# Kernel optimization log

Measured on AMD Instinct MI355X. Metric: run time of the kernel, lower is better.

## Reference

```python
import jax, jax.numpy as jnp
import numpy as np
import math

TANH_CLIP = 10.0
NEG_INF = -100000000.0

def setup_inputs() -> dict:
    key = jax.random.key(0)
    k1, k2, k3, k4, k5 = jax.random.split(key, 5)
    B, Nq, Nk, D = 64, 1024, 1024, 256
    scale = 1.0 / math.sqrt(D)  # ~xavier-ish scale for weights
    return {
        "q": jax.random.normal(k1, (B, Nq, D), dtype=jnp.float32),
        "k": jax.random.normal(k2, (B, Nk, D), dtype=jnp.float32),
        "w_query": jax.random.normal(k3, (D, D), dtype=jnp.float32) * scale,
        "w_key": jax.random.normal(k4, (D, D), dtype=jnp.float32) * scale,
        "mask": jax.random.randint(k5, (B, Nq, Nk), 0, 2, dtype=jnp.int32),
    }

def reference(q, k, w_query, w_key, mask):
    D = q.shape[-1]
    norm = 1.0 / math.sqrt(D)  # key_dim == embedding_dim
    Q = jnp.einsum("bqd,de->bqe", q, w_query)  # [B,Nq,D]
    K = jnp.einsum("bkd,de->bke", k, w_key)    # [B,Nk,D]
    U = norm * jnp.einsum("bqe,bke->bqk", Q, K)
    U = TANH_CLIP * jnp.tanh(U)
    U = jnp.where(mask == 1, NEG_INF, U)
    return jax.nn.log_softmax(U, axis=-1)
```

## Files before the change

### kernel.cpp

```cpp
#include <hip/hip_runtime.h>
#include <hip/hip_bf16.h>
#include <stdint.h>

#define NEG_INF -100000000.0f

typedef __attribute__((ext_vector_type(8))) short bf16x8;
typedef __attribute__((ext_vector_type(4))) float f32x4;
typedef __attribute__((ext_vector_type(4))) int i32x4;

#define LGKM_BAR()                                                \
    do {                                                          \
        asm volatile("s_waitcnt lgkmcnt(0)" ::: "memory");        \
        __builtin_amdgcn_s_barrier();                             \
        __builtin_amdgcn_sched_barrier(0);                        \
    } while (0)

static __device__ __forceinline__ short f2bf(float x) {
    unsigned u = __float_as_uint(x);
    u = u + 0x7FFFu + ((u >> 16) & 1u);
    return (short)(u >> 16);
}

__global__ void wtrans_kernel(const float* __restrict__ wq, const float* __restrict__ wk,
                              short* __restrict__ wtq, short* __restrict__ wtk) {
    __shared__ float tile[32][33];
    const float* w = blockIdx.z ? wk : wq;
    short* wt = blockIdx.z ? wtk : wtq;
    float scale = blockIdx.z ? 1.0f : 0.0625f;
    int tx = threadIdx.x, ty = threadIdx.y;
    int c0 = blockIdx.x * 32;
    int k0 = blockIdx.y * 32;
#pragma unroll
    for (int i = 0; i < 4; i++)
        tile[ty + i * 8][tx] = w[(k0 + ty + i * 8) * 256 + c0 + tx];
    __syncthreads();
#pragma unroll
    for (int i = 0; i < 4; i++)
        wt[(c0 + ty + i * 8) * 256 + k0 + tx] = f2bf(tile[tx][ty + i * 8] * scale);
}

__global__ __launch_bounds__(512, 4)
void proj_kernel(const float* __restrict__ qin, const float* __restrict__ kin,
                 const short* __restrict__ wtq, const short* __restrict__ wtk,
                 short* __restrict__ Qb, short* __restrict__ Kb,
                 const int* __restrict__ mask, unsigned* __restrict__ pmask) {
    if (blockIdx.y == 2) {
        int t = threadIdx.x;
        size_t row = (size_t)blockIdx.x * 64 + (t >> 3);
        int seg8 = t & 7;
        const int* mrow = mask + row * 1024;
#pragma unroll
        for (int jj = 0; jj < 4; jj++) {
            int j = seg8 + jj * 8;
            unsigned v = 0;
#pragma unroll
            for (int i = 0; i < 8; i++) {
                i32x4 x = __builtin_nontemporal_load(
                    reinterpret_cast<const i32x4*>(mrow + j * 4 + i * 128));
                unsigned nib = (unsigned)(x.x | (x.y << 1) | (x.z << 2) | (x.w << 3));
                v |= nib << (i * 4);
            }
            pmask[row * 32 + j] = v;
        }
        return;
    }

    const float* x  = blockIdx.y ? kin : qin;
    const short* wt = blockIdx.y ? wtk : wtq;
    short* outp     = blockIdx.y ? Kb  : Qb;

    __shared__ __align__(16) char slds[40960];
    short* xl0 = (short*)slds;
    short* wl0 = xl0 + 2048;
    short* xl1 = (short*)(slds + 20480);
    short* wl1 = xl1 + 2048;

    int t = threadIdx.x;
    int lane = t & 63, w = t >> 6;
    int l15 = lane & 15, g = lane >> 4;
    int rowbase = blockIdx.x * 64;

    int srow = t >> 3, sseg = t & 7;
    const float* xrow = x + (size_t)(rowbase + srow) * 256 + sseg * 4;
    int wc0 = t >> 2, wseg0 = t & 3;
    int wc1 = (512 + t) >> 2, wseg1 = t & 3;

    f32x4 zero = {0.f, 0.f, 0.f, 0.f};
    f32x4 acc[4][2];
#pragma unroll
    for (int m = 0; m < 4; m++)
#pragma unroll
        for (int n = 0; n < 2; n++) acc[m][n] = zero;

    {
        f32x4 xv = __builtin_nontemporal_load(reinterpret_cast<const f32x4*>(xrow));
        int4 wv0 = *reinterpret_cast<const int4*>(wt + wc0 * 256 + wseg0 * 8);
        int4 wv1 = *reinterpret_cast<const int4*>(wt + wc1 * 256 + wseg1 * 8);
        short4 bb; bb.x = f2bf(xv.x); bb.y = f2bf(xv.y); bb.z = f2bf(xv.z); bb.w = f2bf(xv.w);
        *reinterpret_cast<short4*>(&xl0[srow * 32 + sseg * 4]) = bb;
        *reinterpret_cast<int4*>(&wl0[(size_t)t * 8]) = wv0;
        *reinterpret_cast<int4*>(&wl0[((size_t)512 + t) * 8]) = wv1;
    }
    LGKM_BAR();

#pragma unroll
    for (int dc = 0; dc < 8; dc++) {
        short* xc   = (dc & 1) ? xl1 : xl0;
        short* wcur = (dc & 1) ? wl1 : wl0;
        short* xn   = (dc & 1) ? xl0 : xl1;
        short* wn   = (dc & 1) ? wl0 : wl1;

        f32x4 xv; int4 wv0, wv1;
        if (dc < 7) {
            xv  = __builtin_nontemporal_load(reinterpret_cast<const f32x4*>(xrow + (dc + 1) * 32));
            wv0 = *reinterpret_cast<const int4*>(wt + wc0 * 256 + (dc + 1) * 32 + wseg0 * 8);
            wv1 = *reinterpret_cast<const int4*>(wt + wc1 * 256 + (dc + 1) * 32 + wseg1 * 8);
        }

        bf16x8 a[4], bfr[2];
#pragma unroll
        for (int m = 0; m < 4; m++)
            a[m] = *reinterpret_cast<const bf16x8*>(&xc[(m * 16 + l15) * 32 + g * 8]);
#pragma unroll
        for (int n = 0; n < 2; n++) {
            int c = w * 32 + n * 16 + l15;
            bfr[n] = *reinterpret_cast<const bf16x8*>(&wcur[c * 32 + g * 8]);
        }
#pragma unroll
        for (int m = 0; m < 4; m++)
#pragma unroll
            for (int n = 0; n < 2; n++)
                acc[m][n] = __builtin_amdgcn_mfma_f32_16x16x32_bf16(a[m], bfr[n], acc[m][n], 0, 0, 0);

        if (dc < 7) {
            short4 bb; bb.x = f2bf(xv.x); bb.y = f2bf(xv.y); bb.z = f2bf(xv.z); bb.w = f2bf(xv.w);
            *reinterpret_cast<short4*>(&xn[srow * 32 + sseg * 4]) = bb;
            *reinterpret_cast<int4*>(&wn[(size_t)t * 8]) = wv0;
            *reinterpret_cast<int4*>(&wn[((size_t)512 + t) * 8]) = wv1;
            LGKM_BAR();
        }
    }

    LGKM_BAR();
    short* sdump = (short*)slds;
#pragma unroll
    for (int m = 0; m < 4; m++)
#pragma unroll
        for (int n = 0; n < 2; n++) {
            int col = w * 32 + n * 16 + l15;
#pragma unroll
            for (int r = 0; r < 4; r++)
                sdump[(m * 16 + g * 4 + r) * 296 + col] = f2bf(acc[m][n][r]);
        }
    LGKM_BAR();

    int b8 = rowbase >> 10;
    int rloc = rowbase & 1023;
#pragma unroll
    for (int o = 0; o < 4; o++) {
        int gu = o * 512 + t;
        int dc = gu >> 8;
        int rem = gu & 255;
        int row = rem >> 2, kseg = rem & 3;
        int4 v = *reinterpret_cast<const int4*>(&sdump[row * 296 + dc * 32 + kseg * 8]);
        size_t idx = (((size_t)b8 * 8 + dc) * 1024 + rloc + row) * 32 + kseg * 8;
        *reinterpret_cast<int4*>(outp + idx) = v;
    }
}

__global__ __launch_bounds__(512, 4)
void attn_kernel(const short* __restrict__ Qs, const short* __restrict__ Ks,
                 const unsigned* __restrict__ pmask, float* __restrict__ out) {
    const int RSB = 1034;
    __shared__ __align__(16) short ulds0[16 * RSB];
    __shared__ __align__(16) short ulds1[16 * RSB];

    int t = threadIdx.x;
    int lane = t & 63, w = t >> 6;
    int l15 = lane & 15, g = lane >> 4;

    int bid = blockIdx.x;
    int wg = (bid & 7) * 256 + (bid >> 3);
    int b = wg >> 5;
    int brow = (wg & 31) * 32;

    const unsigned* pm = pmask + ((size_t)b * 1024 + brow) * 32;
    unsigned mw0 = pm[t];
    unsigned mw1 = pm[512 + t];

    const short* qb = Qs + (size_t)b * 8 * 32768;
    const short* kb = Ks + (size_t)b * 8 * 32768;

    f32x4 zero = {0.f, 0.f, 0.f, 0.f};
    f32x4 acc[2][8];
#pragma unroll
    for (int m = 0; m < 2; m++)
#pragma unroll
        for (int n = 0; n < 8; n++) acc[m][n] = zero;

    for (int dc = 0; dc < 8; dc++) {
        const short* qc = qb + dc * 32768;
        const short* kc = kb + dc * 32768;
        bf16x8 a0 = *reinterpret_cast<const bf16x8*>(qc + (brow + l15) * 32 + g * 8);
        bf16x8 a1 = *reinterpret_cast<const bf16x8*>(qc + (brow + 16 + l15) * 32 + g * 8);
#pragma unroll
        for (int n = 0; n < 8; n++) {
            bf16x8 bf = *reinterpret_cast<const bf16x8*>(kc + (w * 128 + n * 16 + l15) * 32 + g * 8);
            acc[0][n] = __builtin_amdgcn_mfma_f32_16x16x32_bf16(a0, bf, acc[0][n], 0, 0, 0);
            acc[1][n] = __builtin_amdgcn_mfma_f32_16x16x32_bf16(a1, bf, acc[1][n], 0, 0, 0);
        }
    }

    int prow = t >> 5;
    int j = t & 31;

#pragma unroll
    for (int n = 0; n < 8; n++)
#pragma unroll
        for (int r = 0; r < 4; r++)
            ulds0[(g * 4 + r) * RSB + w * 128 + n * 16 + l15] = f2bf(acc[0][n][r]);
    LGKM_BAR();

#pragma unroll
    for (int n = 0; n < 8; n++)
#pragma unroll
        for (int r = 0; r < 4; r++)
            ulds1[(g * 4 + r) * RSB + w * 128 + n * 16 + l15] = f2bf(acc[1][n][r]);

#pragma unroll
    for (int m = 0; m < 2; m++) {
        short* buf = m ? ulds1 : ulds0;
        unsigned bits = m ? mw1 : mw0;
        short* urow = buf + prow * RSB;

        float psum = 0.f;
#pragma unroll
        for (int i = 0; i < 8; i++) {
            int col = j * 4 + i * 128;
            unsigned lo = *reinterpret_cast<const unsigned*>(&urow[col]);
            unsigned hi = *reinterpret_cast<const unsigned*>(&urow[col + 2]);
            float uv[4] = {__uint_as_float(lo << 16), __uint_as_float(lo & 0xffff0000u),
                           __uint_as_float(hi << 16), __uint_as_float(hi & 0xffff0000u)};
            unsigned short ucb[4];
#pragma unroll
            for (int c = 0; c < 4; c++) {
                float e2 = __expf(2.0f * uv[c]);
                float tc = 10.0f - 20.0f / (e2 + 1.0f);
                bool msk = (bits >> (i * 4 + c)) & 1;
                float uc = msk ? NEG_INF : tc;
                ucb[c] = (unsigned short)f2bf(uc);
                psum += msk ? 0.0f : __expf(tc);
            }
            *reinterpret_cast<unsigned*>(&urow[col]) = (unsigned)ucb[0] | ((unsigned)ucb[1] << 16);
            *reinterpret_cast<unsigned*>(&urow[col + 2]) = (unsigned)ucb[2] | ((unsigned)ucb[3] << 16);
        }
        psum += __shfl_xor(psum, 1);
        psum += __shfl_xor(psum, 2);
        psum += __shfl_xor(psum, 4);
        psum += __shfl_xor(psum, 8);
        psum += __shfl_xor(psum, 16);
        float lse = __logf(fmaxf(psum, 1e-30f));
        float lse0 = __shfl(lse, 0);
        float lse1 = __shfl(lse, 32);

        float* obase = out + ((size_t)b * 1024 + brow + m * 16) * 1024;
#pragma unroll
        for (int rr = 0; rr < 2; rr++) {
            int r2 = w * 2 + rr;
            float lser = rr ? lse1 : lse0;
            const short* ur2 = buf + r2 * RSB;
            float* orow = obase + (size_t)r2 * 1024;
#pragma unroll
            for (int i2 = 0; i2 < 4; i2++) {
                int col = lane * 4 + i2 * 256;
                unsigned lo = *reinterpret_cast<const unsigned*>(&ur2[col]);
                unsigned hi = *reinterpret_cast<const unsigned*>(&ur2[col + 2]);
                f32x4 o = {__uint_as_float(lo << 16) - lser,
                           __uint_as_float(lo & 0xffff0000u) - lser,
                           __uint_as_float(hi << 16) - lser,
                           __uint_as_float(hi & 0xffff0000u) - lser};
                __builtin_nontemporal_store(o, reinterpret_cast<f32x4*>(orow + col));
            }
        }
        if (m == 0) LGKM_BAR();
    }
}

extern "C" void kernel_launch(void* const* d_in, const int* in_sizes, int n_in,
                              void* d_out, int out_size, void* d_ws, size_t ws_size,
                              hipStream_t stream) {
    const float* q  = (const float*)d_in[0];
    const float* k  = (const float*)d_in[1];
    const float* wq = (const float*)d_in[2];
    const float* wk = (const float*)d_in[3];
    const int* mask = (const int*)d_in[4];
    float* out = (float*)d_out;

    char* ws = (char*)d_ws;
    short* wtq = (short*)ws;
    short* wtk = (short*)(ws + 131072);
    short* Qb  = (short*)(ws + 262144);
    short* Kb  = (short*)(ws + 262144 + 33554432);
    unsigned* pmask = (unsigned*)(ws + 262144 + 2 * 33554432);

    wtrans_kernel<<<dim3(8, 8, 2), dim3(32, 8), 0, stream>>>(wq, wk, wtq, wtk);
    proj_kernel<<<dim3(1024, 3), 512, 0, stream>>>(q, k, wtq, wtk, Qb, Kb, mask, pmask);
    attn_kernel<<<dim3(2048), 512, 0, stream>>>(Qb, Kb, pmask, out);
}
```

Measured before the change: 215.5 us.

## Process four row tiles per block, overlapping next tile's MFMA with softmax epilogue

Each attention block now handles 128 query rows as four 32-row tiles instead of one, cutting the grid from 2048 to 512 blocks. The MFMA matmul for the next tile is interleaved into the tanh/mask/exp loop of the current tile, and the scores are parked in a single combined LDS buffer. The per-row softmax work is remapped to 16 threads per row, with the mask bits loaded as a uint2 per thread. This aims to hide the epilogue's latency behind tensor-core work and to amortize per-block setup. In exchange it puts more registers and LDS on each block, adds two barriers per tile, and leaves fewer blocks to spread across the CUs.

```diff
diff --git a/kernel.cpp b/kernel.cpp
--- a/kernel.cpp
+++ b/kernel.cpp
@@ -171,25 +171,21 @@
 __global__ __launch_bounds__(512, 4)
 void attn_kernel(const short* __restrict__ Qs, const short* __restrict__ Ks,
                  const unsigned* __restrict__ pmask, float* __restrict__ out) {
-    const int RSB = 1034;
-    __shared__ __align__(16) short ulds0[16 * RSB];
-    __shared__ __align__(16) short ulds1[16 * RSB];
+    const int RSB = 1048;
+    __shared__ __align__(16) short park[32 * RSB];
 
     int t = threadIdx.x;
     int lane = t & 63, w = t >> 6;
     int l15 = lane & 15, g = lane >> 4;
+    int prow = t >> 4, j16 = t & 15;
 
     int bid = blockIdx.x;
-    int wg = (bid & 7) * 256 + (bid >> 3);
-    int b = wg >> 5;
-    int brow = (wg & 31) * 32;
-
-    const unsigned* pm = pmask + ((size_t)b * 1024 + brow) * 32;
-    unsigned mw0 = pm[t];
-    unsigned mw1 = pm[512 + t];
-
-    const short* qb = Qs + (size_t)b * 8 * 32768;
-    const short* kb = Ks + (size_t)b * 8 * 32768;
+    int b = (bid & 7) * 8 + ((bid >> 3) >> 3);
+    int brow0 = ((bid >> 3) & 7) * 128;
+
+    const short* qb = Qs + (size_t)b * 262144;
+    const short* kb = Ks + (size_t)b * 262144;
+    const unsigned* pmb = pmask + (size_t)b * 32768;
 
     f32x4 zero = {0.f, 0.f, 0.f, 0.f};
     f32x4 acc[2][8];
@@ -197,12 +193,14 @@
     for (int m = 0; m < 2; m++)
 #pragma unroll
         for (int n = 0; n < 8; n++) acc[m][n] = zero;
+
+    uint2 mw = *reinterpret_cast<const uint2*>(pmb + (size_t)(brow0 + prow) * 32 + j16 * 2);
 
     for (int dc = 0; dc < 8; dc++) {
         const short* qc = qb + dc * 32768;
         const short* kc = kb + dc * 32768;
-        bf16x8 a0 = *reinterpret_cast<const bf16x8*>(qc + (brow + l15) * 32 + g * 8);
-        bf16x8 a1 = *reinterpret_cast<const bf16x8*>(qc + (brow + 16 + l15) * 32 + g * 8);
+        bf16x8 a0 = *reinterpret_cast<const bf16x8*>(qc + (brow0 + l15) * 32 + g * 8);
+        bf16x8 a1 = *reinterpret_cast<const bf16x8*>(qc + (brow0 + 16 + l15) * 32 + g * 8);
 #pragma unroll
         for (int n = 0; n < 8; n++) {
             bf16x8 bf = *reinterpret_cast<const bf16x8*>(kc + (w * 128 + n * 16 + l15) * 32 + g * 8);
@@ -210,71 +208,85 @@
             acc[1][n] = __builtin_amdgcn_mfma_f32_16x16x32_bf16(a1, bf, acc[1][n], 0, 0, 0);
         }
     }
-
-    int prow = t >> 5;
-    int j = t & 31;
-
-#pragma unroll
-    for (int n = 0; n < 8; n++)
-#pragma unroll
-        for (int r = 0; r < 4; r++)
-            ulds0[(g * 4 + r) * RSB + w * 128 + n * 16 + l15] = f2bf(acc[0][n][r]);
+#pragma unroll
+    for (int m = 0; m < 2; m++)
+#pragma unroll
+        for (int n = 0; n < 8; n++) {
+#pragma unroll
+            for (int r = 0; r < 4; r++)
+                park[(m * 16 + g * 4 + r) * RSB + w * 128 + n * 16 + l15] = f2bf(acc[m][n][r]);
+            acc[m][n] = zero;
+        }
     LGKM_BAR();
 
-#pragma unroll
-    for (int n = 0; n < 8; n++)
-#pragma unroll
-        for (int r = 0; r < 4; r++)
-            ulds1[(g * 4 + r) * RSB + w * 128 + n * 16 + l15] = f2bf(acc[1][n][r]);
-
-#pragma unroll
-    for (int m = 0; m < 2; m++) {
-        short* buf = m ? ulds1 : ulds0;
-        unsigned bits = m ? mw1 : mw0;
-        short* urow = buf + prow * RSB;
+    for (int i = 0; i < 4; ++i) {
+        int brow_i = brow0 + i * 32;
+        int brow_n = brow_i + 32;
+        uint2 mwn;
+        if (i < 3)
+            mwn = *reinterpret_cast<const uint2*>(pmb + (size_t)(brow_n + prow) * 32 + j16 * 2);
 
         float psum = 0.f;
-#pragma unroll
-        for (int i = 0; i < 8; i++) {
-            int col = j * 4 + i * 128;
-            unsigned lo = *reinterpret_cast<const unsigned*>(&urow[col]);
-            unsigned hi = *reinterpret_cast<const unsigned*>(&urow[col + 2]);
-            float uv[4] = {__uint_as_float(lo << 16), __uint_as_float(lo & 0xffff0000u),
-                           __uint_as_float(hi << 16), __uint_as_float(hi & 0xffff0000u)};
-            unsigned short ucb[4];
-#pragma unroll
-            for (int c = 0; c < 4; c++) {
-                float e2 = __expf(2.0f * uv[c]);
-                float tc = 10.0f - 20.0f / (e2 + 1.0f);
-                bool msk = (bits >> (i * 4 + c)) & 1;
-                float uc = msk ? NEG_INF : tc;
-                ucb[c] = (unsigned short)f2bf(uc);
-                psum += msk ? 0.0f : __expf(tc);
+        short* urow = park + prow * RSB;
+        for (int dc = 0; dc < 8; ++dc) {
+            if (i < 3) {
+                const short* qc = qb + dc * 32768;
+                const short* kc = kb + dc * 32768;
+                bf16x8 a0 = *reinterpret_cast<const bf16x8*>(qc + (brow_n + l15) * 32 + g * 8);
+                bf16x8 a1 = *reinterpret_cast<const bf16x8*>(qc + (brow_n + 16 + l15) * 32 + g * 8);
+#pragma unroll
+                for (int n = 0; n < 8; n++) {
+                    bf16x8 bf = *reinterpret_cast<const bf16x8*>(kc + (w * 128 + n * 16 + l15) * 32 + g * 8);
+                    acc[0][n] = __builtin_amdgcn_mfma_f32_16x16x32_bf16(a0, bf, acc[0][n], 0, 0, 0);
+                    acc[1][n] = __builtin_amdgcn_mfma_f32_16x16x32_bf16(a1, bf, acc[1][n], 0, 0, 0);
+                }
             }
-            *reinterpret_cast<unsigned*>(&urow[col]) = (unsigned)ucb[0] | ((unsigned)ucb[1] << 16);
-            *reinterpret_cast<unsigned*>(&urow[col + 2]) = (unsigned)ucb[2] | ((unsigned)ucb[3] << 16);
-        }
+            int c0 = j16 * 8 + dc * 128;
+            i32x4 raw = *reinterpret_cast<const i32x4*>(urow + c0);
+            unsigned blo = (mw.x >> (dc * 4)) & 0xFu;
+            unsigned bhi = (mw.y >> (dc * 4)) & 0xFu;
+            unsigned rw0 = (unsigned)raw.x, rw1 = (unsigned)raw.y;
+            unsigned rw2 = (unsigned)raw.z, rw3 = (unsigned)raw.w;
+            unsigned ow[4];
+            unsigned rws[4] = {rw0, rw1, rw2, rw3};
+#pragma unroll
+            for (int h = 0; h < 4; h++) {
+                float u0 = __uint_as_float(rws[h] << 16);
+                float u1 = __uint_as_float(rws[h] & 0xffff0000u);
+                unsigned bb2 = (h < 2) ? (blo >> (h * 2)) : (bhi >> ((h - 2) * 2));
+                float e20 = __expf(2.0f * u0), e21 = __expf(2.0f * u1);
+                float t0 = 10.0f - 20.0f / (e20 + 1.0f);
+                float t1 = 10.0f - 20.0f / (e21 + 1.0f);
+                bool m0 = bb2 & 1, m1 = (bb2 >> 1) & 1;
+                float uc0 = m0 ? NEG_INF : t0;
+                float uc1 = m1 ? NEG_INF : t1;
+                psum += m0 ? 0.0f : __expf(t0);
+                psum += m1 ? 0.0f : __expf(t1);
+                ow[h] = ((unsigned)(unsigned short)f2bf(uc0)) |
+                        (((unsigned)(unsigned short)f2bf(uc1)) << 16);
+            }
+            i32x4 o = {(int)ow[0], (int)ow[1], (int)ow[2], (int)ow[3]};
+            *reinterpret_cast<i32x4*>(urow + c0) = o;
+        }
+
         psum += __shfl_xor(psum, 1);
         psum += __shfl_xor(psum, 2);
         psum += __shfl_xor(psum, 4);
         psum += __shfl_xor(psum, 8);
-        psum += __shfl_xor(psum, 16);
         float lse = __logf(fmaxf(psum, 1e-30f));
-        float lse0 = __shfl(lse, 0);
-        float lse1 = __shfl(lse, 32);
-
-        float* obase = out + ((size_t)b * 1024 + brow + m * 16) * 1024;
-#pragma unroll
-        for (int rr = 0; rr < 2; rr++) {
-            int r2 = w * 2 + rr;
-            float lser = rr ? lse1 : lse0;
-            const short* ur2 = buf + r2 * RSB;
+
+        float* obase = out + ((size_t)b * 1024 + brow_i) * 1024;
+#pragma unroll
+        for (int rr = 0; rr < 4; rr++) {
+            int r2 = w * 4 + rr;
+            float lser = __shfl(lse, rr * 16);
+            const short* ur2 = park + r2 * RSB;
             float* orow = obase + (size_t)r2 * 1024;
 #pragma unroll
-            for (int i2 = 0; i2 < 4; i2++) {
-                int col = lane * 4 + i2 * 256;
-                unsigned lo = *reinterpret_cast<const unsigned*>(&ur2[col]);
-                unsigned hi = *reinterpret_cast<const unsigned*>(&ur2[col + 2]);
+            for (int seg = 0; seg < 4; seg++) {
+                int col = lane * 4 + seg * 256;
+                unsigned lo = *reinterpret_cast<const unsigned*>(ur2 + col);
+                unsigned hi = *reinterpret_cast<const unsigned*>(ur2 + col + 2);
                 f32x4 o = {__uint_as_float(lo << 16) - lser,
                            __uint_as_float(lo & 0xffff0000u) - lser,
                            __uint_as_float(hi << 16) - lser,
@@ -282,7 +294,21 @@
                 __builtin_nontemporal_store(o, reinterpret_cast<f32x4*>(orow + col));
             }
         }
-        if (m == 0) LGKM_BAR();
+
+        LGKM_BAR();
+        if (i < 3) {
+#pragma unroll
+            for (int m = 0; m < 2; m++)
+#pragma unroll
+                for (int n = 0; n < 8; n++) {
+#pragma unroll
+                    for (int r = 0; r < 4; r++)
+                        park[(m * 16 + g * 4 + r) * RSB + w * 128 + n * 16 + l15] = f2bf(acc[m][n][r]);
+                    acc[m][n] = zero;
+                }
+            mw = mwn;
+        }
+        LGKM_BAR();
     }
 }
 
@@ -305,5 +331,5 @@
 
     wtrans_kernel<<<dim3(8, 8, 2), dim3(32, 8), 0, stream>>>(wq, wk, wtq, wtk);
     proj_kernel<<<dim3(1024, 3), 512, 0, stream>>>(q, k, wtq, wtk, Qb, Kb, mask, pmask);
-    attn_kernel<<<dim3(2048), 512, 0, stream>>>(Qb, Kb, pmask, out);
-}
+    attn_kernel<<<dim3(512), 512, 0, stream>>>(Qb, Kb, pmask, out);
+}
```

Result: slower. 255.4 us (+18.5%).

## Apply tanh/mask/exp in MFMA register layout and pre-swizzle packed mask

Applied to the files above, without the earlier changes.

The mask-packing blocks now transpose the packed bits through LDS so that each thread's mask word matches the MFMA accumulator layout. The attention kernel can then compute tanh, masking and exp directly on accumulator registers. Row sums are reduced with shuffles plus a small LDS reduction buffer instead of a second LDS read-modify-write pass. This removes one LDS round trip and one barrier, and it computes tanh in fp32 before rounding to bf16. In exchange, the mask packing pass gets more work and the attention kernel uses a single larger LDS buffer.

```diff
diff --git a/kernel.cpp b/kernel.cpp
--- a/kernel.cpp
+++ b/kernel.cpp
@@ -44,11 +44,14 @@
                  const short* __restrict__ wtq, const short* __restrict__ wtk,
                  short* __restrict__ Qb, short* __restrict__ Kb,
                  const int* __restrict__ mask, unsigned* __restrict__ pmask) {
+    __shared__ __align__(16) char slds[40960];
+
     if (blockIdx.y == 2) {
+        unsigned* words = (unsigned*)slds;
         int t = threadIdx.x;
-        size_t row = (size_t)blockIdx.x * 64 + (t >> 3);
-        int seg8 = t & 7;
-        const int* mrow = mask + row * 1024;
+        int row = t >> 3, seg8 = t & 7;
+        size_t grow = (size_t)blockIdx.x * 64 + row;
+        const int* mrow = mask + grow * 1024;
 #pragma unroll
         for (int jj = 0; jj < 4; jj++) {
             int j = seg8 + jj * 8;
@@ -60,8 +63,30 @@
                 unsigned nib = (unsigned)(x.x | (x.y << 1) | (x.z << 2) | (x.w << 3));
                 v |= nib << (i * 4);
             }
-            pmask[row * 32 + j] = v;
-        }
+            words[row * 33 + j] = v;
+        }
+        __syncthreads();
+        int w_o = t >> 6, lane_o = t & 63;
+        int g_o = lane_o >> 4, l15 = lane_o & 15;
+        int bitpos = w_o * 4 + (l15 & 3);
+        int jb = l15 >> 2;
+        unsigned* obase = pmask + (size_t)blockIdx.x * 2048;
+#pragma unroll
+        for (int tt = 0; tt < 2; tt++)
+#pragma unroll
+            for (int mm = 0; mm < 2; mm++) {
+                unsigned v = 0;
+#pragma unroll
+                for (int r = 0; r < 4; r++) {
+                    int rrow = tt * 32 + mm * 16 + g_o * 4 + r;
+#pragma unroll
+                    for (int n = 0; n < 8; n++) {
+                        unsigned bit = (words[rrow * 33 + n * 4 + jb] >> bitpos) & 1u;
+                        v |= bit << (r * 8 + n);
+                    }
+                }
+                obase[tt * 1024 + mm * 512 + t] = v;
+            }
         return;
     }
 
@@ -69,7 +94,6 @@
     const short* wt = blockIdx.y ? wtk : wtq;
     short* outp     = blockIdx.y ? Kb  : Qb;
 
-    __shared__ __align__(16) char slds[40960];
     short* xl0 = (short*)slds;
     short* wl0 = xl0 + 2048;
     short* xl1 = (short*)(slds + 20480);
@@ -170,10 +194,10 @@
 
 __global__ __launch_bounds__(512, 4)
 void attn_kernel(const short* __restrict__ Qs, const short* __restrict__ Ks,
-                 const unsigned* __restrict__ pmask, float* __restrict__ out) {
+                 const unsigned* __restrict__ pmf, float* __restrict__ out) {
     const int RSB = 1034;
-    __shared__ __align__(16) short ulds0[16 * RSB];
-    __shared__ __align__(16) short ulds1[16 * RSB];
+    __shared__ __align__(16) short park[32 * RSB];
+    __shared__ float redbuf[32 * 8];
 
     int t = threadIdx.x;
     int lane = t & 63, w = t >> 6;
@@ -182,9 +206,10 @@
     int bid = blockIdx.x;
     int wg = (bid & 7) * 256 + (bid >> 3);
     int b = wg >> 5;
-    int brow = (wg & 31) * 32;
-
-    const unsigned* pm = pmask + ((size_t)b * 1024 + brow) * 32;
+    int qt = wg & 31;
+    int brow = qt * 32;
+
+    const unsigned* pm = pmf + (size_t)(b * 32 + qt) * 1024;
     unsigned mw0 = pm[t];
     unsigned mw1 = pm[512 + t];
 
@@ -211,68 +236,63 @@
         }
     }
 
-    int prow = t >> 5;
-    int j = t & 31;
-
-#pragma unroll
-    for (int n = 0; n < 8; n++)
-#pragma unroll
-        for (int r = 0; r < 4; r++)
-            ulds0[(g * 4 + r) * RSB + w * 128 + n * 16 + l15] = f2bf(acc[0][n][r]);
+    float rowsum[2][4];
+#pragma unroll
+    for (int m = 0; m < 2; m++)
+#pragma unroll
+        for (int r = 0; r < 4; r++) rowsum[m][r] = 0.f;
+
+#pragma unroll
+    for (int m = 0; m < 2; m++) {
+        unsigned bits = m ? mw1 : mw0;
+#pragma unroll
+        for (int n = 0; n < 8; n++)
+#pragma unroll
+            for (int r = 0; r < 4; r++) {
+                float u = acc[m][n][r];
+                float e2 = __expf(2.0f * u);
+                float tc = 10.0f - 20.0f / (e2 + 1.0f);
+                bool msk = (bits >> (r * 8 + n)) & 1;
+                float uc = msk ? NEG_INF : tc;
+                rowsum[m][r] += msk ? 0.0f : __expf(tc);
+                park[(m * 16 + g * 4 + r) * RSB + w * 128 + n * 16 + l15] = f2bf(uc);
+            }
+    }
+
+#pragma unroll
+    for (int m = 0; m < 2; m++)
+#pragma unroll
+        for (int r = 0; r < 4; r++) {
+            float s = rowsum[m][r];
+            s += __shfl_xor(s, 1);
+            s += __shfl_xor(s, 2);
+            s += __shfl_xor(s, 4);
+            s += __shfl_xor(s, 8);
+            rowsum[m][r] = s;
+        }
+    if (l15 == 0) {
+#pragma unroll
+        for (int m = 0; m < 2; m++)
+#pragma unroll
+            for (int r = 0; r < 4; r++)
+                redbuf[(m * 16 + g * 4 + r) * 8 + w] = rowsum[m][r];
+    }
     LGKM_BAR();
 
 #pragma unroll
-    for (int n = 0; n < 8; n++)
-#pragma unroll
-        for (int r = 0; r < 4; r++)
-            ulds1[(g * 4 + r) * RSB + w * 128 + n * 16 + l15] = f2bf(acc[1][n][r]);
-
-#pragma unroll
-    for (int m = 0; m < 2; m++) {
-        short* buf = m ? ulds1 : ulds0;
-        unsigned bits = m ? mw1 : mw0;
-        short* urow = buf + prow * RSB;
-
-        float psum = 0.f;
-#pragma unroll
-        for (int i = 0; i < 8; i++) {
-            int col = j * 4 + i * 128;
-            unsigned lo = *reinterpret_cast<const unsigned*>(&urow[col]);
-            unsigned hi = *reinterpret_cast<const unsigned*>(&urow[col + 2]);
-            float uv[4] = {__uint_as_float(lo << 16), __uint_as_float(lo & 0xffff0000u),
-                           __uint_as_float(hi << 16), __uint_as_float(hi & 0xffff0000u)};
-            unsigned short ucb[4];
-#pragma unroll
-            for (int c = 0; c < 4; c++) {
-                float e2 = __expf(2.0f * uv[c]);
-                float tc = 10.0f - 20.0f / (e2 + 1.0f);
-                bool msk = (bits >> (i * 4 + c)) & 1;
-                float uc = msk ? NEG_INF : tc;
-                ucb[c] = (unsigned short)f2bf(uc);
-                psum += msk ? 0.0f : __expf(tc);
-            }
-            *reinterpret_cast<unsigned*>(&urow[col]) = (unsigned)ucb[0] | ((unsigned)ucb[1] << 16);
-            *reinterpret_cast<unsigned*>(&urow[col + 2]) = (unsigned)ucb[2] | ((unsigned)ucb[3] << 16);
-        }
-        psum += __shfl_xor(psum, 1);
-        psum += __shfl_xor(psum, 2);
-        psum += __shfl_xor(psum, 4);
-        psum += __shfl_xor(psum, 8);
-        psum += __shfl_xor(psum, 16);
-        float lse = __logf(fmaxf(psum, 1e-30f));
-        float lse0 = __shfl(lse, 0);
-        float lse1 = __shfl(lse, 32);
-
-        float* obase = out + ((size_t)b * 1024 + brow + m * 16) * 1024;
+    for (int m = 0; m < 2; m++)
 #pragma unroll
         for (int rr = 0; rr < 2; rr++) {
-            int r2 = w * 2 + rr;
-            float lser = rr ? lse1 : lse0;
-            const short* ur2 = buf + r2 * RSB;
-            float* orow = obase + (size_t)r2 * 1024;
-#pragma unroll
-            for (int i2 = 0; i2 < 4; i2++) {
-                int col = lane * 4 + i2 * 256;
+            int pr = m * 16 + w * 2 + rr;
+            const float4* rb = reinterpret_cast<const float4*>(&redbuf[pr * 8]);
+            float4 s0 = rb[0], s1 = rb[1];
+            float ssum = ((s0.x + s0.y) + (s0.z + s0.w)) + ((s1.x + s1.y) + (s1.z + s1.w));
+            float lser = __logf(fmaxf(ssum, 1e-30f));
+            const short* ur2 = park + pr * RSB;
+            float* orow = out + ((size_t)b * 1024 + brow + pr) * 1024;
+#pragma unroll
+            for (int seg = 0; seg < 4; seg++) {
+                int col = lane * 4 + seg * 256;
                 unsigned lo = *reinterpret_cast<const unsigned*>(&ur2[col]);
                 unsigned hi = *reinterpret_cast<const unsigned*>(&ur2[col + 2]);
                 f32x4 o = {__uint_as_float(lo << 16) - lser,
@@ -282,8 +302,6 @@
                 __builtin_nontemporal_store(o, reinterpret_cast<f32x4*>(orow + col));
             }
         }
-        if (m == 0) LGKM_BAR();
-    }
 }
 
 extern "C" void kernel_launch(void* const* d_in, const int* in_sizes, int n_in,
```

After: 220.5 us. 2.3% more time.
